# Kernel optimization log

Hardware: AMD Instinct MI355X
Metric: run time of the kernel (lower is better)

Reference implementation:

```python
import jax, jax.numpy as jnp
import numpy as np

N_CLASSES = 150
N_PRED = 8192
GAMMA = 4.0
IGNORE_INDEX = 0


def _norm_factor(gamma, eps=1e-7):
    # (gamma+1) / trapz((1 - t**(gamma+1)) / (1 - t), t) on t in [0, 1-eps], 1000 pts
    t = jnp.linspace(0.0, 1.0 - eps, 1000)
    y = (1.0 - t ** (gamma + 1.0)) / (1.0 - t)
    h = jnp.sum(0.5 * (y[1:] + y[:-1]) * (t[1:] - t[:-1]))
    return (gamma + 1.0) / h


def setup_inputs() -> dict:
    key = jax.random.key(0)
    k1, k2, k3 = jax.random.split(key, 3)
    B, H, W = 16, 1024, 1024
    pred = jax.random.normal(k1, (N_PRED, N_CLASSES), dtype=jnp.float32)
    predseg = jax.random.randint(k2, (B, H, W), 0, N_PRED, dtype=jnp.int32)
    targetseg = jax.random.randint(k3, (B, H, W), 0, N_CLASSES, dtype=jnp.int32)
    return {"pred": pred, "predseg": predseg, "targetseg": targetseg}


def reference(pred, predseg, targetseg):
    P, C = pred.shape            # num pred segments, n_classes
    B = predseg.shape[0]
    T = B * C                    # combined target id space (b*n_classes + cls)

    p = predseg.reshape(-1)                                          # [Npix]
    cls = targetseg.reshape(-1)                                      # [Npix]
    b = jnp.broadcast_to(
        jnp.arange(B, dtype=p.dtype).reshape(B, 1, 1), predseg.shape
    ).reshape(-1)
    t = b * C + cls                                                  # combined target id
    pair = p * T + t                                                 # unique (pred, target) pair key

    ones = jnp.ones(p.shape, dtype=jnp.float32)
    # histogram counts, gathered back per-pixel
    n_ov = jnp.zeros((P * T,), jnp.float32).at[pair].add(ones)[pair]  # overlap count of pixel's pair
    n_p = jnp.zeros((P,), jnp.float32).at[p].add(ones)[p]             # pred segment size
    n_t = jnp.zeros((T,), jnp.float32).at[t].add(ones)[t]             # target segment size

    # Each unique pair contributes iou = n_ov/(n_p+n_t-n_ov) once; summing per pixel
    # the weight iou/n_ov == 1/(n_p+n_t-n_ov) reproduces the scatter_reduce of ious.
    w = 1.0 / (n_p + n_t - n_ov)
    out = jnp.zeros((P, C), jnp.float32).at[p, cls].add(w)
    target = out / jnp.sum(out, axis=-1, keepdims=True)

    cls_w = jnp.ones((C,), jnp.float32).at[IGNORE_INDEX].set(0.0)
    logp = jax.nn.log_softmax(pred, axis=-1)
    ce = -jnp.sum(cls_w * target * logp, axis=-1)                     # weighted soft-label CE
    pt = jnp.take_along_axis(
        jax.nn.softmax(pred, axis=-1),
        jnp.argmax(target, axis=-1, keepdims=True),
        axis=-1,
    )[:, 0]
    c = _norm_factor(GAMMA)
    loss = (1.0 - pt) ** GAMMA * ce * c
    return jnp.mean(loss)
```

## Files before the change

kernel.cpp:

```cpp
#include <hip/hip_runtime.h>
#include <math.h>

#define N_PRED   8192
#define N_CLS    150
#define N_BATCH  16
#define T_DIM    (N_BATCH * N_CLS)
#define NPIX     (N_BATCH * 1024 * 1024)
#define PIX_SHIFT 20

#define STRIPE   16384
#define NBLK_A   (NPIX / STRIPE)
#define NBUK     512
#define P_PER_BUK 16

#define KEYS_BYTES ((size_t)NPIX * 2)
#define DIRT_BYTES ((size_t)NBUK * NBLK_A * 4)
#define NT_BYTES   ((size_t)T_DIM * 4)

__global__ __launch_bounds__(1024, 8) void partition_kernel(
    const int* __restrict__ predseg, const int* __restrict__ targetseg,
    unsigned short* __restrict__ keys, unsigned* __restrict__ dirT,
    unsigned* __restrict__ g_nt) {
    __shared__ unsigned s_cnt[NBUK];
    __shared__ unsigned s_sa[NBUK];
    __shared__ unsigned s_wsum[8];
    __shared__ unsigned s_nt[N_CLS];
    __shared__ unsigned short s_keys[STRIPE];

    int tid = threadIdx.x;
    int blk = blockIdx.x;
    size_t base = (size_t)blk * STRIPE;
    int tbase = (int)(base >> PIX_SHIFT) * N_CLS;

    if (tid < NBUK)  s_cnt[tid] = 0u;
    if (tid < N_CLS) s_nt[tid]  = 0u;
    __syncthreads();

    const int4* pv4 = (const int4*)(predseg   + base);
    const int4* cv4 = (const int4*)(targetseg + base);

    unsigned kreg[16];
    #pragma unroll
    for (int i = 0; i < 4; ++i) {
        int idx = tid + i * 1024;
        int4 pv = pv4[idx]; int4 cv = cv4[idx];
        unsigned w0 = ((unsigned)pv.x << 12) | (unsigned)(tbase + cv.x);
        unsigned w1 = ((unsigned)pv.y << 12) | (unsigned)(tbase + cv.y);
        unsigned w2 = ((unsigned)pv.z << 12) | (unsigned)(tbase + cv.z);
        unsigned w3 = ((unsigned)pv.w << 12) | (unsigned)(tbase + cv.w);
        kreg[4 * i]     = w0; kreg[4 * i + 1] = w1;
        kreg[4 * i + 2] = w2; kreg[4 * i + 3] = w3;
        atomicAdd(&s_cnt[w0 >> 16], 1u); atomicAdd(&s_cnt[w1 >> 16], 1u);
        atomicAdd(&s_cnt[w2 >> 16], 1u); atomicAdd(&s_cnt[w3 >> 16], 1u);
        atomicAdd(&s_nt[cv.x], 1u); atomicAdd(&s_nt[cv.y], 1u);
        atomicAdd(&s_nt[cv.z], 1u); atomicAdd(&s_nt[cv.w], 1u);
    }
    __syncthreads();

    int lane = tid & 63;
    if (tid < NBUK) {
        unsigned x = s_cnt[tid];
        #pragma unroll
        for (int d = 1; d < 64; d <<= 1) {
            unsigned y = __shfl_up(x, d, 64);
            if (lane >= d) x += y;
        }
        if (lane == 63) s_wsum[tid >> 6] = x;
        s_sa[tid] = x;
    }
    __syncthreads();
    if (tid < 8) {
        unsigned v = s_wsum[tid];
        #pragma unroll
        for (int d = 1; d < 8; d <<= 1) {
            unsigned y = __shfl_up(v, d, 8);
            if ((tid & 7) >= d) v += y;
        }
        s_wsum[tid] = v;
    }
    __syncthreads();

    if (tid < NBUK) {
        unsigned wofs = (tid >= 64) ? s_wsum[(tid >> 6) - 1] : 0u;
        unsigned incl = s_sa[tid] + wofs;
        unsigned cnt  = s_cnt[tid];
        unsigned excl = incl - cnt;
        dirT[(size_t)tid * NBLK_A + blk] = excl | (cnt << 16);
        s_cnt[tid] = excl;
    }
    __syncthreads();

    #pragma unroll
    for (int i = 0; i < 16; ++i) {
        unsigned w = kreg[i];
        unsigned slot = atomicAdd(&s_cnt[w >> 16], 1u);
        s_keys[slot] = (unsigned short)w;
    }
    __syncthreads();

    uint4* dstv = (uint4*)(keys + base);
    const uint4* srcv = (const uint4*)s_keys;
    #pragma unroll
    for (int i = 0; i < 2; ++i) dstv[tid + i * 1024] = srcv[tid + i * 1024];

    if (tid < N_CLS) {
        unsigned v = s_nt[tid];
        if (v) atomicAdd(&g_nt[tbase + tid], v);
    }
}

__global__ __launch_bounds__(1024, 8) void hist_loss_kernel(
    const unsigned short* __restrict__ keys, const unsigned* __restrict__ dirT,
    const unsigned* __restrict__ g_nt, const float* __restrict__ pred,
    float* __restrict__ loss_out, float cnorm) {
    __shared__ unsigned s_hist[P_PER_BUK * T_DIM / 4];
    __shared__ unsigned s_dir[NBLK_A];
    __shared__ float s_ntf[T_DIM];
    __shared__ float s_loss[P_PER_BUK];

    int tid = threadIdx.x;
    int q   = blockIdx.x;
    for (int i = tid; i < P_PER_BUK * T_DIM / 4; i += 1024) s_hist[i] = 0u;
    s_dir[tid] = dirT[(size_t)q * NBLK_A + tid];
    for (int i = tid; i < T_DIM; i += 1024) s_ntf[i] = (float)g_nt[i];
    __syncthreads();

    int wid  = tid >> 6;
    int lane = tid & 63;
    int g    = lane >> 4;
    int u    = lane & 15;

    for (int s = wid * 4 + g; s < NBLK_A; s += 64) {
        unsigned d = s_dir[s];
        int start = (int)(d & 0xFFFFu);
        int cnt   = (int)(d >> 16);
        if (!cnt) continue;
        int end = start + cnt;
        const unsigned* kw = (const unsigned*)(keys + (size_t)s * STRIPE);
        int w0 = start >> 1;
        int w1 = (end - 1) >> 1;
        for (int w = w0 + u; w <= w1; w += 16) {
            unsigned x = kw[w];
            if (2 * w >= start) {
                unsigned k = x & 0xFFFFu;
                unsigned bin = (k >> 12) * T_DIM + (k & 4095u);
                atomicAdd(&s_hist[bin >> 2], 1u << ((bin & 3u) * 8));
            }
            if (2 * w + 1 < end) {
                unsigned k = x >> 16;
                unsigned bin = (k >> 12) * T_DIM + (k & 4095u);
                atomicAdd(&s_hist[bin >> 2], 1u << ((bin & 3u) * 8));
            }
        }
    }
    __syncthreads();

    float np;
    {
        unsigned sum = 0;
        const unsigned* row = s_hist + wid * (T_DIM / 4);
        for (int t = lane; t < T_DIM / 4; t += 64) {
            unsigned w = row[t];
            sum += (w & 0xFFu) + ((w >> 8) & 0xFFu) + ((w >> 16) & 0xFFu) + (w >> 24);
        }
        #pragma unroll
        for (int off = 32; off; off >>= 1) sum += __shfl_xor(sum, off);
        np = (float)sum;
    }

    const float* pr = pred + (size_t)(q * P_PER_BUK + wid) * N_CLS;
    float pv[3], ov[3];
    float rowsum = 0.f, pmax = -INFINITY;
    #pragma unroll
    for (int k = 0; k < 3; ++k) {
        int c = lane + k * 64;
        bool ok = c < N_CLS;
        pv[k] = ok ? pr[c] : -INFINITY;
        float acc = 0.f;
        if (ok) {
            #pragma unroll
            for (int b = 0; b < N_BATCH; ++b) {
                int t = b * N_CLS + c;
                unsigned bin = (unsigned)(wid * T_DIM + t);
                unsigned cb = (s_hist[bin >> 2] >> ((bin & 3u) * 8)) & 0xFFu;
                if (cb) {
                    float f = (float)cb;
                    acc += f / (np + s_ntf[t] - f);
                }
            }
        }
        ov[k] = acc;
        rowsum += acc;
        pmax = fmaxf(pmax, pv[k]);
    }
    #pragma unroll
    for (int off = 32; off; off >>= 1) {
        rowsum += __shfl_xor(rowsum, off);
        pmax = fmaxf(pmax, __shfl_xor(pmax, off));
    }
    float sumexp = 0.f;
    #pragma unroll
    for (int k = 0; k < 3; ++k) {
        int c = lane + k * 64;
        if (c < N_CLS) sumexp += __expf(pv[k] - pmax);
    }
    #pragma unroll
    for (int off = 32; off; off >>= 1) sumexp += __shfl_xor(sumexp, off);
    float lse = __logf(sumexp) + pmax;

    float inv = 1.f / rowsum;
    float ce = 0.f, bestv = -INFINITY;
    int besti = 0;
    #pragma unroll
    for (int k = 0; k < 3; ++k) {
        int c = lane + k * 64;
        if (c >= N_CLS) continue;
        float tg = ov[k] * inv;
        if (c != 0) ce -= tg * (pv[k] - lse);
        if (tg > bestv) { bestv = tg; besti = c; }
    }
    #pragma unroll
    for (int off = 32; off; off >>= 1) {
        ce += __shfl_xor(ce, off);
        float bv = __shfl_xor(bestv, off);
        int   bi = __shfl_xor(besti, off);
        if (bv > bestv || (bv == bestv && bi < besti)) { bestv = bv; besti = bi; }
    }
    if (lane == 0) {
        float ptv = __expf(pr[besti] - lse);
        float x  = 1.f - ptv;
        float x2 = x * x;
        s_loss[wid] = x2 * x2 * ce * cnorm;
    }
    __syncthreads();
    if (tid == 0) {
        float s = 0.f;
        #pragma unroll
        for (int r = 0; r < P_PER_BUK; ++r) s += s_loss[r];
        atomicAdd(loss_out, s * (1.0f / (float)N_PRED));
    }
}

static float compute_cnorm() {
    const double eps = 1e-7, gamma = 4.0;
    double h = 0.0, prev_t = 0.0, prev_y = 1.0;
    for (int i = 1; i < 1000; ++i) {
        double t = (double)i * (1.0 - eps) / 999.0;
        double y = (1.0 - pow(t, gamma + 1.0)) / (1.0 - t);
        h += 0.5 * (y + prev_y) * (t - prev_t);
        prev_t = t; prev_y = y;
    }
    return (float)((gamma + 1.0) / h);
}

extern "C" void kernel_launch(void* const* d_in, const int* in_sizes, int n_in,
                              void* d_out, int out_size, void* d_ws, size_t ws_size,
                              hipStream_t stream) {
    const float* pred      = (const float*)d_in[0];
    const int*   predseg   = (const int*)d_in[1];
    const int*   targetseg = (const int*)d_in[2];

    unsigned char* ws = (unsigned char*)d_ws;
    unsigned short* keys = (unsigned short*)ws;
    unsigned* dirT = (unsigned*)(ws + KEYS_BYTES);
    unsigned* g_nt = (unsigned*)(ws + KEYS_BYTES + DIRT_BYTES);

    float cnorm = compute_cnorm();

    hipMemsetAsync(g_nt, 0, NT_BYTES, stream);
    hipMemsetAsync(d_out, 0, sizeof(float) * (size_t)out_size, stream);

    partition_kernel<<<NBLK_A, 1024, 0, stream>>>(predseg, targetseg, keys, dirT, g_nt);
    hist_loss_kernel<<<NBUK,   1024, 0, stream>>>(keys, dirT, g_nt, pred,
                                                  (float*)d_out, cnorm);
}
```

Baseline: 82.43 us.

## Split histogram and loss into separate kernels, derive target counts from histograms

Removes the per-pixel target-class shared atomics from the partition kernel. Each histogram block now sums its byte histogram over its 16 predictions to produce per-target counts, adds them to the global target-count array, and writes the histogram to workspace. A third kernel reloads the histograms and computes the loss. The extra launch and the global round trip of about 20 MB of histograms are traded against lighter partition work, and the old two-kernel path is kept as a fallback when the workspace is too small.

Result: slower. 97.00 us (+17.7%).

```diff
diff --git a/kernel.cpp b/kernel.cpp
--- a/kernel.cpp
+++ b/kernel.cpp
@@ -13,10 +13,13 @@
 #define NBUK     512
 #define P_PER_BUK 16
 
-#define KEYS_BYTES ((size_t)NPIX * 2)
-#define DIRT_BYTES ((size_t)NBUK * NBLK_A * 4)
-#define NT_BYTES   ((size_t)T_DIM * 4)
-
+#define KEYS_BYTES  ((size_t)NPIX * 2)
+#define DIRT_BYTES  ((size_t)NBUK * NBLK_A * 4)
+#define NT_BYTES    ((size_t)T_DIM * 4)
+#define GHIST_BYTES ((size_t)NBUK * P_PER_BUK * T_DIM)
+#define WS_NEED_3K  (KEYS_BYTES + DIRT_BYTES + NT_BYTES + GHIST_BYTES)
+
+template<bool WITH_NT>
 __global__ __launch_bounds__(1024, 8) void partition_kernel(
     const int* __restrict__ predseg, const int* __restrict__ targetseg,
     unsigned short* __restrict__ keys, unsigned* __restrict__ dirT,
@@ -32,8 +35,8 @@
     size_t base = (size_t)blk * STRIPE;
     int tbase = (int)(base >> PIX_SHIFT) * N_CLS;
 
-    if (tid < NBUK)  s_cnt[tid] = 0u;
-    if (tid < N_CLS) s_nt[tid]  = 0u;
+    if (tid < NBUK) s_cnt[tid] = 0u;
+    if (WITH_NT && tid < N_CLS) s_nt[tid] = 0u;
     __syncthreads();
 
     const int4* pv4 = (const int4*)(predseg   + base);
@@ -52,8 +55,10 @@
         kreg[4 * i + 2] = w2; kreg[4 * i + 3] = w3;
         atomicAdd(&s_cnt[w0 >> 16], 1u); atomicAdd(&s_cnt[w1 >> 16], 1u);
         atomicAdd(&s_cnt[w2 >> 16], 1u); atomicAdd(&s_cnt[w3 >> 16], 1u);
-        atomicAdd(&s_nt[cv.x], 1u); atomicAdd(&s_nt[cv.y], 1u);
-        atomicAdd(&s_nt[cv.z], 1u); atomicAdd(&s_nt[cv.w], 1u);
+        if (WITH_NT) {
+            atomicAdd(&s_nt[cv.x], 1u); atomicAdd(&s_nt[cv.y], 1u);
+            atomicAdd(&s_nt[cv.z], 1u); atomicAdd(&s_nt[cv.w], 1u);
+        }
     }
     __syncthreads();
 
@@ -103,33 +108,23 @@
     #pragma unroll
     for (int i = 0; i < 2; ++i) dstv[tid + i * 1024] = srcv[tid + i * 1024];
 
-    if (tid < N_CLS) {
+    if (WITH_NT && tid < N_CLS) {
         unsigned v = s_nt[tid];
         if (v) atomicAdd(&g_nt[tbase + tid], v);
     }
 }
 
-__global__ __launch_bounds__(1024, 8) void hist_loss_kernel(
+__device__ __forceinline__ void build_hist(
     const unsigned short* __restrict__ keys, const unsigned* __restrict__ dirT,
-    const unsigned* __restrict__ g_nt, const float* __restrict__ pred,
-    float* __restrict__ loss_out, float cnorm) {
-    __shared__ unsigned s_hist[P_PER_BUK * T_DIM / 4];
-    __shared__ unsigned s_dir[NBLK_A];
-    __shared__ float s_ntf[T_DIM];
-    __shared__ float s_loss[P_PER_BUK];
-
-    int tid = threadIdx.x;
-    int q   = blockIdx.x;
+    unsigned* s_hist, unsigned* s_dir, int tid, int q) {
     for (int i = tid; i < P_PER_BUK * T_DIM / 4; i += 1024) s_hist[i] = 0u;
     s_dir[tid] = dirT[(size_t)q * NBLK_A + tid];
-    for (int i = tid; i < T_DIM; i += 1024) s_ntf[i] = (float)g_nt[i];
     __syncthreads();
 
     int wid  = tid >> 6;
     int lane = tid & 63;
     int g    = lane >> 4;
     int u    = lane & 15;
-
     for (int s = wid * 4 + g; s < NBLK_A; s += 64) {
         unsigned d = s_dir[s];
         int start = (int)(d & 0xFFFFu);
@@ -154,7 +149,14 @@
         }
     }
     __syncthreads();
-
+}
+
+__device__ __forceinline__ void loss_epilogue(
+    const unsigned* s_hist, const float* s_ntf, float* s_loss,
+    const float* __restrict__ pred, float* __restrict__ loss_out,
+    float cnorm, int tid, int q) {
+    int wid  = tid >> 6;
+    int lane = tid & 63;
     float np;
     {
         unsigned sum = 0;
@@ -241,6 +243,65 @@
     }
 }
 
+__global__ __launch_bounds__(1024, 8) void hist_store_kernel(
+    const unsigned short* __restrict__ keys, const unsigned* __restrict__ dirT,
+    unsigned* __restrict__ g_nt, unsigned char* __restrict__ ghist) {
+    __shared__ unsigned s_hist[P_PER_BUK * T_DIM / 4];
+    __shared__ unsigned s_dir[NBLK_A];
+
+    int tid = threadIdx.x;
+    int q   = blockIdx.x;
+    build_hist(keys, dirT, s_hist, s_dir, tid, q);
+
+    for (int t = tid; t < T_DIM; t += 1024) {
+        unsigned sum = 0;
+        #pragma unroll
+        for (int lp = 0; lp < P_PER_BUK; ++lp) {
+            unsigned bin = (unsigned)(lp * T_DIM + t);
+            sum += (s_hist[bin >> 2] >> ((bin & 3u) * 8)) & 0xFFu;
+        }
+        if (sum) atomicAdd(&g_nt[t], sum);
+    }
+
+    uint4* dst = (uint4*)(ghist + (size_t)q * (P_PER_BUK * T_DIM));
+    const uint4* src = (const uint4*)s_hist;
+    for (int i = tid; i < P_PER_BUK * T_DIM / 16; i += 1024) dst[i] = src[i];
+}
+
+__global__ __launch_bounds__(1024, 8) void loss_from_hist_kernel(
+    const unsigned char* __restrict__ ghist, const unsigned* __restrict__ g_nt,
+    const float* __restrict__ pred, float* __restrict__ loss_out, float cnorm) {
+    __shared__ unsigned s_hist[P_PER_BUK * T_DIM / 4];
+    __shared__ float s_ntf[T_DIM];
+    __shared__ float s_loss[P_PER_BUK];
+
+    int tid = threadIdx.x;
+    int q   = blockIdx.x;
+    const uint4* src = (const uint4*)(ghist + (size_t)q * (P_PER_BUK * T_DIM));
+    uint4* dst = (uint4*)s_hist;
+    for (int i = tid; i < P_PER_BUK * T_DIM / 16; i += 1024) dst[i] = src[i];
+    for (int i = tid; i < T_DIM; i += 1024) s_ntf[i] = (float)g_nt[i];
+    __syncthreads();
+
+    loss_epilogue(s_hist, s_ntf, s_loss, pred, loss_out, cnorm, tid, q);
+}
+
+__global__ __launch_bounds__(1024, 8) void hist_loss_kernel(
+    const unsigned short* __restrict__ keys, const unsigned* __restrict__ dirT,
+    const unsigned* __restrict__ g_nt, const float* __restrict__ pred,
+    float* __restrict__ loss_out, float cnorm) {
+    __shared__ unsigned s_hist[P_PER_BUK * T_DIM / 4];
+    __shared__ unsigned s_dir[NBLK_A];
+    __shared__ float s_ntf[T_DIM];
+    __shared__ float s_loss[P_PER_BUK];
+
+    int tid = threadIdx.x;
+    int q   = blockIdx.x;
+    for (int i = tid; i < T_DIM; i += 1024) s_ntf[i] = (float)g_nt[i];
+    build_hist(keys, dirT, s_hist, s_dir, tid, q);
+    loss_epilogue(s_hist, s_ntf, s_loss, pred, loss_out, cnorm, tid, q);
+}
+
 static float compute_cnorm() {
     const double eps = 1e-7, gamma = 4.0;
     double h = 0.0, prev_t = 0.0, prev_y = 1.0;
@@ -264,13 +325,23 @@
     unsigned short* keys = (unsigned short*)ws;
     unsigned* dirT = (unsigned*)(ws + KEYS_BYTES);
     unsigned* g_nt = (unsigned*)(ws + KEYS_BYTES + DIRT_BYTES);
+    unsigned char* ghist = ws + KEYS_BYTES + DIRT_BYTES + NT_BYTES;
 
     float cnorm = compute_cnorm();
 
     hipMemsetAsync(g_nt, 0, NT_BYTES, stream);
     hipMemsetAsync(d_out, 0, sizeof(float) * (size_t)out_size, stream);
 
-    partition_kernel<<<NBLK_A, 1024, 0, stream>>>(predseg, targetseg, keys, dirT, g_nt);
-    hist_loss_kernel<<<NBUK,   1024, 0, stream>>>(keys, dirT, g_nt, pred,
-                                                  (float*)d_out, cnorm);
-}
+    if (ws_size >= WS_NEED_3K) {
+        partition_kernel<false><<<NBLK_A, 1024, 0, stream>>>(
+            predseg, targetseg, keys, dirT, g_nt);
+        hist_store_kernel<<<NBUK, 1024, 0, stream>>>(keys, dirT, g_nt, ghist);
+        loss_from_hist_kernel<<<NBUK, 1024, 0, stream>>>(
+            ghist, g_nt, pred, (float*)d_out, cnorm);
+    } else {
+        partition_kernel<true><<<NBLK_A, 1024, 0, stream>>>(
+            predseg, targetseg, keys, dirT, g_nt);
+        hist_loss_kernel<<<NBUK, 1024, 0, stream>>>(
+            keys, dirT, g_nt, pred, (float*)d_out, cnorm);
+    }
+}
```
